# Kernel tuning notes

Hardware: AMD Instinct MI355X
Metric: run time of the kernel (lower is better)

The kernel has to match this reference:

```python
import jax, jax.numpy as jnp
import numpy as np

NCLASS = 21  # num_classes from init
EPS = 1e-6


def setup_inputs() -> dict:
    key = jax.random.key(0)
    k1, k2 = jax.random.split(key)
    feats = jax.random.normal(k1, (8, 256, 64, 64), dtype=jnp.float32)
    masks = jax.random.randint(k2, (8, 256, 256), 0, NCLASS, dtype=jnp.int32)
    return {"feats": feats, "masks": masks}


def reference(feats, masks):
    # feats: [B, C, h, w] float; masks: [B, H, W] int labels
    B, C, _, _ = feats.shape
    H, W = masks.shape[-2:]
    # F.interpolate(..., mode='bilinear', align_corners=False) == half-pixel bilinear resize
    f = jax.image.resize(feats, (B, C, H, W), method="bilinear")  # [B,C,H,W]
    f_flat = f.reshape(B, C, H * W)  # [B,C,P]

    # labels > nclass (e.g. 255 ignore) are clamped to the dump bucket `nclass`;
    # pixels with label == nclass are excluded (one_hot drops out-of-range rows).
    lbl = jnp.where(masks > NCLASS, NCLASS, masks).reshape(B, H * W)  # [B,P]
    onehot = jax.nn.one_hot(lbl, NCLASS, dtype=f.dtype)  # [B,P,K], dump bucket -> all zeros

    # segment-reduce: per-image per-class feature sums and pixel counts
    sums = jnp.einsum("bcp,bpk->bkc", f_flat, onehot)  # [B,K,C]
    counts = onehot.sum(axis=1)  # [B,K]
    per_img = sums / (counts[..., None] + EPS)  # [B,K,C]; absent classes -> ~0, matching torch loop skip
    prototypes = per_img.mean(axis=0)  # [K,C] (sum over batch / b)
    return prototypes
```

## Files before the change

### kernel.cpp

```cpp
#include <hip/hip_runtime.h>

#define NK 21
#define NC 256
#define NSRC 64
#define NOUT 256
#define NB 8
#define NSL 256
#define NG 8
#define EPS 1e-6f

__device__ __forceinline__ void lds_fadd(float* p, float v) {
  __hip_atomic_fetch_add(p, v, __ATOMIC_RELAXED, __HIP_MEMORY_SCOPE_WORKGROUP);
}

__global__ __launch_bounds__(256, 4)
void proto_main(const float* __restrict__ feats,
                const int* __restrict__ masks,
                float* __restrict__ psum,
                float* __restrict__ pcnt) {
  __shared__ __align__(16) float Wl[NK * 16];
  __shared__ int hist[NK];

  const int tid = threadIdx.x;
  const int r0 = blockIdx.x;
  const int b = blockIdx.y;
  const int z = blockIdx.z;

  const float4* fbase = (const float4*)(
      feats + ((size_t)(b * NC + tid) << 12) + (size_t)r0 * 64 + 16 * z);
  const float4 f0 = fbase[0], f1 = fbase[1], f2 = fbase[2], f3 = fbase[3];

  for (int i = tid; i < NK * 16; i += 256) Wl[i] = 0.f;
  if (tid < NK) hist[tid] = 0;
  __syncthreads();

  const int ylo = 4 * r0 - 2;
  const int xbase = 64 * z - 2;
  for (int i = tid; i < 544; i += 256) {
    const int x = xbase + i % 68;
    const int y = ylo + i / 68;
    if ((unsigned)(x | y) < 256u) {
      const int lbl = masks[((size_t)b * NOUT + y) * NOUT + x];
      if ((unsigned)lbl < NK) {
        const int ry = y >> 2, py = y & 3;
        const int j0y = (py < 2) ? ry - 1 : ry;
        const float fy = (py == 0) ? 0.625f : (py == 1) ? 0.875f
                       : (py == 2) ? 0.125f : 0.375f;
        const int rx = x >> 2, px = x & 3;
        const int j0x = (px < 2) ? rx - 1 : rx;
        const float fx = (px == 0) ? 0.625f : (px == 1) ? 0.875f
                       : (px == 2) ? 0.125f : 0.375f;

        const int cx0 = (j0x < 0) ? 0 : j0x;
        const int cx1 = (j0x + 1 > NSRC - 1) ? NSRC - 1 : j0x + 1;
        const float wx0 = 1.f - fx, wx1 = fx;
        const int ry0 = (j0y < 0) ? 0 : j0y;
        const int ry1 = (j0y + 1 > NSRC - 1) ? NSRC - 1 : j0y + 1;
        const float wy0 = 1.f - fy, wy1 = fy;

        float* Wk = &Wl[lbl * 16];
        if (ry0 == r0) {
          if ((cx0 >> 4) == z) lds_fadd(&Wk[cx0 & 15], wy0 * wx0);
          if ((cx1 >> 4) == z) lds_fadd(&Wk[cx1 & 15], wy0 * wx1);
        }
        if (ry1 == r0) {
          if ((cx0 >> 4) == z) lds_fadd(&Wk[cx0 & 15], wy1 * wx0);
          if ((cx1 >> 4) == z) lds_fadd(&Wk[cx1 & 15], wy1 * wx1);
        }
        if (y >= 4 * r0 && y < 4 * r0 + 4 && (x >> 6) == z)
          atomicAdd(&hist[lbl], 1);
      }
    }
  }
  __syncthreads();

  float acc[NK];
  const float4* wb = (const float4*)Wl;
#pragma unroll
  for (int k = 0; k < NK; ++k) {
    const float4 w0 = wb[k * 4 + 0], w1 = wb[k * 4 + 1];
    const float4 w2 = wb[k * 4 + 2], w3 = wb[k * 4 + 3];
    float a = 0.f;
    a = fmaf(f0.x, w0.x, a); a = fmaf(f0.y, w0.y, a);
    a = fmaf(f0.z, w0.z, a); a = fmaf(f0.w, w0.w, a);
    a = fmaf(f1.x, w1.x, a); a = fmaf(f1.y, w1.y, a);
    a = fmaf(f1.z, w1.z, a); a = fmaf(f1.w, w1.w, a);
    a = fmaf(f2.x, w2.x, a); a = fmaf(f2.y, w2.y, a);
    a = fmaf(f2.z, w2.z, a); a = fmaf(f2.w, w2.w, a);
    a = fmaf(f3.x, w3.x, a); a = fmaf(f3.y, w3.y, a);
    a = fmaf(f3.z, w3.z, a); a = fmaf(f3.w, w3.w, a);
    acc[k] = a;
  }

  const int sl = r0 * 4 + z;
  float* dst = psum + ((size_t)(b * NSL + sl) * NK) * NC + tid;
#pragma unroll
  for (int k = 0; k < NK; ++k) dst[k * NC] = acc[k];
  if (tid < NK) pcnt[(size_t)(b * NSL + sl) * NK + tid] = (float)hist[tid];
}

__global__ __launch_bounds__(256)
void proto_finalA(const float* __restrict__ psum,
                  const float* __restrict__ pcnt,
                  float* __restrict__ psum2,
                  float* __restrict__ pcnt2) {
  const int k = blockIdx.x;
  const int b = blockIdx.y;
  const int g = blockIdx.z;
  const int c = threadIdx.x;
  const int sl0 = g * 32;
  float s = 0.f, cnt = 0.f;
#pragma unroll
  for (int j = 0; j < 32; ++j) {
    s += psum[((size_t)(b * NSL + sl0 + j) * NK + k) * NC + c];
    cnt += pcnt[(size_t)(b * NSL + sl0 + j) * NK + k];
  }
  psum2[((size_t)(b * NG + g) * NK + k) * NC + c] = s;
  if (c == 0) pcnt2[(size_t)(b * NG + g) * NK + k] = cnt;
}

__global__ __launch_bounds__(256)
void proto_finalB(const float* __restrict__ psum2,
                  const float* __restrict__ pcnt2,
                  float* __restrict__ out) {
  const int k = blockIdx.x;
  const int c = threadIdx.x;
  float a = 0.f;
#pragma unroll
  for (int b = 0; b < NB; ++b) {
    float s = 0.f, cnt = 0.f;
#pragma unroll
    for (int g = 0; g < NG; ++g) {
      s += psum2[((size_t)(b * NG + g) * NK + k) * NC + c];
      cnt += pcnt2[(size_t)(b * NG + g) * NK + k];
    }
    a += s / (cnt + EPS);
  }
  out[(size_t)k * NC + c] = a * 0.125f;
}

extern "C" void kernel_launch(void* const* d_in, const int* in_sizes, int n_in,
                              void* d_out, int out_size, void* d_ws, size_t ws_size,
                              hipStream_t stream) {
  const float* feats = (const float*)d_in[0];
  const int* masks = (const int*)d_in[1];
  float* out = (float*)d_out;

  float* psum = (float*)d_ws;
  float* pcnt = psum + (size_t)NB * NSL * NK * NC;
  float* psum2 = pcnt + (size_t)NB * NSL * NK;
  float* pcnt2 = psum2 + (size_t)NB * NG * NK * NC;

  proto_main<<<dim3(64, NB, 4), 256, 0, stream>>>(feats, masks, psum, pcnt);
  proto_finalA<<<dim3(NK, NB, NG), 256, 0, stream>>>(psum, pcnt, psum2, pcnt2);
  proto_finalB<<<dim3(NK), 256, 0, stream>>>(psum2, pcnt2, out);
}
```

Measured before the change: 104.2 us.

## Split fused kernel into mask-scatter and feature-apply kernels over full rows

```diff
diff --git a/kernel.cpp b/kernel.cpp
--- a/kernel.cpp
+++ b/kernel.cpp
@@ -5,7 +5,6 @@
 #define NSRC 64
 #define NOUT 256
 #define NB 8
-#define NSL 256
 #define NG 8
 #define EPS 1e-6f
 
@@ -13,90 +12,102 @@
   __hip_atomic_fetch_add(p, v, __ATOMIC_RELAXED, __HIP_MEMORY_SCOPE_WORKGROUP);
 }
 
-__global__ __launch_bounds__(256, 4)
-void proto_main(const float* __restrict__ feats,
-                const int* __restrict__ masks,
-                float* __restrict__ psum,
-                float* __restrict__ pcnt) {
-  __shared__ __align__(16) float Wl[NK * 16];
+__global__ __launch_bounds__(256)
+void proto_scatter(const int* __restrict__ masks,
+                   float* __restrict__ Wg,
+                   float* __restrict__ pcnt) {
+  __shared__ float Wl[NK * 64];
   __shared__ int hist[NK];
 
   const int tid = threadIdx.x;
   const int r0 = blockIdx.x;
   const int b = blockIdx.y;
-  const int z = blockIdx.z;
 
-  const float4* fbase = (const float4*)(
-      feats + ((size_t)(b * NC + tid) << 12) + (size_t)r0 * 64 + 16 * z);
-  const float4 f0 = fbase[0], f1 = fbase[1], f2 = fbase[2], f3 = fbase[3];
-
-  for (int i = tid; i < NK * 16; i += 256) Wl[i] = 0.f;
+  for (int i = tid; i < NK * 64; i += 256) Wl[i] = 0.f;
   if (tid < NK) hist[tid] = 0;
   __syncthreads();
 
-  const int ylo = 4 * r0 - 2;
-  const int xbase = 64 * z - 2;
-  for (int i = tid; i < 544; i += 256) {
-    const int x = xbase + i % 68;
-    const int y = ylo + i / 68;
-    if ((unsigned)(x | y) < 256u) {
-      const int lbl = masks[((size_t)b * NOUT + y) * NOUT + x];
-      if ((unsigned)lbl < NK) {
-        const int ry = y >> 2, py = y & 3;
-        const int j0y = (py < 2) ? ry - 1 : ry;
-        const float fy = (py == 0) ? 0.625f : (py == 1) ? 0.875f
-                       : (py == 2) ? 0.125f : 0.375f;
-        const int rx = x >> 2, px = x & 3;
-        const int j0x = (px < 2) ? rx - 1 : rx;
-        const float fx = (px == 0) ? 0.625f : (px == 1) ? 0.875f
-                       : (px == 2) ? 0.125f : 0.375f;
+  int ylo = 4 * r0 - 2; if (ylo < 0) ylo = 0;
+  int yhi = 4 * r0 + 5; if (yhi > NOUT - 1) yhi = NOUT - 1;
+  const int npix = (yhi - ylo + 1) * NOUT;
+  const int own_lo = 4 * r0;
 
-        const int cx0 = (j0x < 0) ? 0 : j0x;
-        const int cx1 = (j0x + 1 > NSRC - 1) ? NSRC - 1 : j0x + 1;
-        const float wx0 = 1.f - fx, wx1 = fx;
-        const int ry0 = (j0y < 0) ? 0 : j0y;
-        const int ry1 = (j0y + 1 > NSRC - 1) ? NSRC - 1 : j0y + 1;
-        const float wy0 = 1.f - fy, wy1 = fy;
+  for (int i = tid; i < npix; i += 256) {
+    const int x = i & (NOUT - 1);
+    const int y = ylo + (i >> 8);
+    const int lbl = masks[((size_t)b * NOUT + y) * NOUT + x];
+    if ((unsigned)lbl < NK) {
+      const int ry = y >> 2, py = y & 3;
+      const int j0y = (py < 2) ? ry - 1 : ry;
+      const float fy = (py == 0) ? 0.625f : (py == 1) ? 0.875f
+                     : (py == 2) ? 0.125f : 0.375f;
+      const int rx = x >> 2, px = x & 3;
+      const int j0x = (px < 2) ? rx - 1 : rx;
+      const float fx = (px == 0) ? 0.625f : (px == 1) ? 0.875f
+                     : (px == 2) ? 0.125f : 0.375f;
 
-        float* Wk = &Wl[lbl * 16];
-        if (ry0 == r0) {
-          if ((cx0 >> 4) == z) lds_fadd(&Wk[cx0 & 15], wy0 * wx0);
-          if ((cx1 >> 4) == z) lds_fadd(&Wk[cx1 & 15], wy0 * wx1);
-        }
-        if (ry1 == r0) {
-          if ((cx0 >> 4) == z) lds_fadd(&Wk[cx0 & 15], wy1 * wx0);
-          if ((cx1 >> 4) == z) lds_fadd(&Wk[cx1 & 15], wy1 * wx1);
-        }
-        if (y >= 4 * r0 && y < 4 * r0 + 4 && (x >> 6) == z)
-          atomicAdd(&hist[lbl], 1);
+      const int cx0 = (j0x < 0) ? 0 : j0x;
+      const int cx1 = (j0x + 1 > NSRC - 1) ? NSRC - 1 : j0x + 1;
+      const float wx0 = 1.f - fx, wx1 = fx;
+      const int ry0 = (j0y < 0) ? 0 : j0y;
+      const int ry1 = (j0y + 1 > NSRC - 1) ? NSRC - 1 : j0y + 1;
+      const float wy0 = 1.f - fy, wy1 = fy;
+
+      float* Wk = &Wl[lbl * 64];
+      if (ry0 == r0) {
+        lds_fadd(&Wk[cx0], wy0 * wx0);
+        lds_fadd(&Wk[cx1], wy0 * wx1);
       }
+      if (ry1 == r0) {
+        lds_fadd(&Wk[cx0], wy1 * wx0);
+        lds_fadd(&Wk[cx1], wy1 * wx1);
+      }
+      if (y >= own_lo && y < own_lo + 4) atomicAdd(&hist[lbl], 1);
     }
   }
   __syncthreads();
 
+  float* wdst = Wg + (size_t)(b * 64 + r0) * (NK * 64);
+  for (int i = tid; i < NK * 64; i += 256) wdst[i] = Wl[i];
+  if (tid < NK) pcnt[(size_t)(b * 64 + r0) * NK + tid] = (float)hist[tid];
+}
+
+__global__ __launch_bounds__(256, 4)
+void proto_apply(const float* __restrict__ feats,
+                 const float* __restrict__ Wg,
+                 float* __restrict__ psum) {
+  const int tid = threadIdx.x;
+  const int r0 = blockIdx.x;
+  const int b = blockIdx.y;
+
+  const int woff4 = __builtin_amdgcn_readfirstlane((b * 64 + r0) * (NK * 16));
+  const float4* __restrict__ w4 = (const float4*)Wg + woff4;
+
+  const float4* fbase =
+      (const float4*)(feats + ((size_t)(b * NC + tid) << 12) + (size_t)r0 * 64);
+  float4 f[16];
+#pragma unroll
+  for (int j = 0; j < 16; ++j) f[j] = fbase[j];
+
   float acc[NK];
-  const float4* wb = (const float4*)Wl;
 #pragma unroll
   for (int k = 0; k < NK; ++k) {
-    const float4 w0 = wb[k * 4 + 0], w1 = wb[k * 4 + 1];
-    const float4 w2 = wb[k * 4 + 2], w3 = wb[k * 4 + 3];
+    const float4* wk = w4 + k * 16;
     float a = 0.f;
-    a = fmaf(f0.x, w0.x, a); a = fmaf(f0.y, w0.y, a);
-    a = fmaf(f0.z, w0.z, a); a = fmaf(f0.w, w0.w, a);
-    a = fmaf(f1.x, w1.x, a); a = fmaf(f1.y, w1.y, a);
-    a = fmaf(f1.z, w1.z, a); a = fmaf(f1.w, w1.w, a);
-    a = fmaf(f2.x, w2.x, a); a = fmaf(f2.y, w2.y, a);
-    a = fmaf(f2.z, w2.z, a); a = fmaf(f2.w, w2.w, a);
-    a = fmaf(f3.x, w3.x, a); a = fmaf(f3.y, w3.y, a);
-    a = fmaf(f3.z, w3.z, a); a = fmaf(f3.w, w3.w, a);
+#pragma unroll
+    for (int j = 0; j < 16; ++j) {
+      const float4 w = wk[j];
+      a = fmaf(f[j].x, w.x, a);
+      a = fmaf(f[j].y, w.y, a);
+      a = fmaf(f[j].z, w.z, a);
+      a = fmaf(f[j].w, w.w, a);
+    }
     acc[k] = a;
   }
 
-  const int sl = r0 * 4 + z;
-  float* dst = psum + ((size_t)(b * NSL + sl) * NK) * NC + tid;
+  float* dst = psum + ((size_t)(b * 64 + r0) * NK) * NC + tid;
 #pragma unroll
   for (int k = 0; k < NK; ++k) dst[k * NC] = acc[k];
-  if (tid < NK) pcnt[(size_t)(b * NSL + sl) * NK + tid] = (float)hist[tid];
 }
 
 __global__ __launch_bounds__(256)
@@ -108,12 +119,12 @@
   const int b = blockIdx.y;
   const int g = blockIdx.z;
   const int c = threadIdx.x;
-  const int sl0 = g * 32;
+  const int r0 = g * 8;
   float s = 0.f, cnt = 0.f;
 #pragma unroll
-  for (int j = 0; j < 32; ++j) {
-    s += psum[((size_t)(b * NSL + sl0 + j) * NK + k) * NC + c];
-    cnt += pcnt[(size_t)(b * NSL + sl0 + j) * NK + k];
+  for (int j = 0; j < 8; ++j) {
+    s += psum[((size_t)(b * 64 + r0 + j) * NK + k) * NC + c];
+    cnt += pcnt[(size_t)(b * 64 + r0 + j) * NK + k];
   }
   psum2[((size_t)(b * NG + g) * NK + k) * NC + c] = s;
   if (c == 0) pcnt2[(size_t)(b * NG + g) * NK + k] = cnt;
@@ -146,12 +157,14 @@
   const int* masks = (const int*)d_in[1];
   float* out = (float*)d_out;
 
-  float* psum = (float*)d_ws;
-  float* pcnt = psum + (size_t)NB * NSL * NK * NC;
-  float* psum2 = pcnt + (size_t)NB * NSL * NK;
+  float* Wg = (float*)d_ws;
+  float* psum = Wg + (size_t)NB * 64 * NK * 64;
+  float* pcnt = psum + (size_t)NB * 64 * NK * NC;
+  float* psum2 = pcnt + (size_t)NB * 64 * NK;
   float* pcnt2 = psum2 + (size_t)NB * NG * NK * NC;
 
-  proto_main<<<dim3(64, NB, 4), 256, 0, stream>>>(feats, masks, psum, pcnt);
+  proto_scatter<<<dim3(64, NB), 256, 0, stream>>>(masks, Wg, pcnt);
+  proto_apply<<<dim3(64, NB), 256, 0, stream>>>(feats, Wg, psum);
   proto_finalA<<<dim3(NK, NB, NG), 256, 0, stream>>>(psum, pcnt, psum2, pcnt2);
   proto_finalB<<<dim3(NK), 256, 0, stream>>>(psum2, pcnt2, out);
 }
```

Result: slower. 107.6 us (+3.2%).
